# Kernel optimization log

Hardware: AMD Instinct MI355X
Metric: run time of the kernel (lower is better)

Reference implementation:

```python
import jax, jax.numpy as jnp
import numpy as np

M, N = 32, 32
IN_MULT, OUT_MULT = 5, 40
HQ = M * M  # 1024, hidden size of GRU_Q and GRU_Sigma; GRU_S hidden = N*N = 1024


def _l2norm(x):
    # torch F.normalize(p=2, dim=0, eps=1e-12)
    return x / jnp.maximum(jnp.linalg.norm(x), 1e-12)


def _gru(x, h, Wih, Whh, bih, bhh):
    # single-step torch nn.GRU cell, gate order r,z,n
    gi = Wih @ x + bih
    gh = Whh @ h + bhh
    Hh = h.shape[0]
    r = jax.nn.sigmoid(gi[:Hh] + gh[:Hh])
    z = jax.nn.sigmoid(gi[Hh:2 * Hh] + gh[Hh:2 * Hh])
    n = jnp.tanh(gi[2 * Hh:] + r * gh[2 * Hh:])
    return (1.0 - z) * n + z * h


def setup_inputs() -> dict:
    key = jax.random.key(0)
    ks = iter(jax.random.split(key, 48))

    def rn(shape, scale=1.0):
        return jax.random.normal(next(ks), shape, dtype=jnp.float32) * jnp.float32(scale)

    def w(o, i):
        return rn((o, i), 1.0 / np.sqrt(i))

    d_in_sigma = HQ + M * IN_MULT          # 1184
    d_in_s = N * N + 2 * N * IN_MULT       # 1344
    d_fc2_in = HQ + N * N                  # 2048
    d_fc2_hid = d_fc2_in * OUT_MULT        # 81920
    inp = dict(
        y=rn((N,)),
        m1x_posterior=rn((M, 1)), m1x_posterior_previous=rn((M, 1)),
        m1x_prior_previous=rn((M, 1)), y_previous=rn((N, 1)),
        h_Q=rn((HQ,)), h_Sigma=rn((HQ,)), h_S=rn((N * N,)),
        F=w(M, M), H=w(N, M),
        FC5_w=w(M * IN_MULT, M), FC5_b=rn((M * IN_MULT,), 0.01),
        FC6_w=w(M * IN_MULT, M), FC6_b=rn((M * IN_MULT,), 0.01),
        FC7_w=w(2 * N * IN_MULT, 2 * N), FC7_b=rn((2 * N * IN_MULT,), 0.01),
        GRUQ_Wih=w(3 * HQ, M * IN_MULT), GRUQ_Whh=w(3 * HQ, HQ),
        GRUQ_bih=rn((3 * HQ,), 0.01), GRUQ_bhh=rn((3 * HQ,), 0.01),
        GRUSig_Wih=w(3 * HQ, d_in_sigma), GRUSig_Whh=w(3 * HQ, HQ),
        GRUSig_bih=rn((3 * HQ,), 0.01), GRUSig_bhh=rn((3 * HQ,), 0.01),
        GRUS_Wih=w(3 * N * N, d_in_s), GRUS_Whh=w(3 * N * N, N * N),
        GRUS_bih=rn((3 * N * N,), 0.01), GRUS_bhh=rn((3 * N * N,), 0.01),
        FC1_w=w(N * N, HQ), FC1_b=rn((N * N,), 0.01),
        FC2_w1=w(d_fc2_hid, d_fc2_in), FC2_b1=rn((d_fc2_hid,), 0.01),
        FC2_w2=w(N * M, d_fc2_hid), FC2_b2=rn((N * M,), 0.01),
        FC3_w=w(M * M, N * N + N * M), FC3_b=rn((M * M,), 0.01),
        FC4_w=w(HQ, HQ + M * M), FC4_b=rn((HQ,), 0.01),
        fix_H_flag=1,
    )
    return inp


def _forward(y, m1x_posterior, m1x_posterior_previous, m1x_prior_previous, y_previous,
             h_Q, h_Sigma, h_S, F, H,
             FC5_w, FC5_b, FC6_w, FC6_b, FC7_w, FC7_b,
             GRUQ_Wih, GRUQ_Whh, GRUQ_bih, GRUQ_bhh,
             GRUSig_Wih, GRUSig_Whh, GRUSig_bih, GRUSig_bhh,
             GRUS_Wih, GRUS_Whh, GRUS_bih, GRUS_bhh,
             FC1_w, FC1_b, FC2_w1, FC2_b1, FC2_w2, FC2_b2,
             FC3_w, FC3_b, FC4_w, FC4_b):
    # step_prior (fix_H_flag=True path: h is linear)
    m1x_prior = F @ m1x_posterior          # [m,1]
    m1y = H @ m1x_prior                    # [n,1]
    # step_KGain_est: feature differences, L2-normalized
    obs_diff = _l2norm(y - y_previous[:, 0])
    obs_innov_diff = _l2norm(y - m1y[:, 0])
    fw_evol_diff = _l2norm(m1x_posterior[:, 0] - m1x_posterior_previous[:, 0])
    fw_update_diff = _l2norm(m1x_posterior[:, 0] - m1x_prior_previous[:, 0])
    # KGain_step (dropout layers are identity in eval)
    out_FC5 = jax.nn.relu(FC5_w @ fw_evol_diff + FC5_b)
    out_Q = _gru(out_FC5, h_Q, GRUQ_Wih, GRUQ_Whh, GRUQ_bih, GRUQ_bhh)
    out_FC6 = jax.nn.relu(FC6_w @ fw_update_diff + FC6_b)
    out_Sigma = _gru(jnp.concatenate([out_Q, out_FC6]), h_Sigma,
                     GRUSig_Wih, GRUSig_Whh, GRUSig_bih, GRUSig_bhh)
    out_FC1 = jax.nn.relu(FC1_w @ out_Sigma + FC1_b)
    out_FC7 = jax.nn.relu(FC7_w @ jnp.concatenate([obs_diff, obs_innov_diff]) + FC7_b)
    out_S = _gru(jnp.concatenate([out_FC1, out_FC7]), h_S,
                 GRUS_Wih, GRUS_Whh, GRUS_bih, GRUS_bhh)
    in_FC2 = jnp.concatenate([out_Sigma, out_S])
    out_FC2 = FC2_w2 @ jax.nn.relu(FC2_w1 @ in_FC2 + FC2_b1) + FC2_b2   # [m*n]
    out_FC3 = jax.nn.relu(FC3_w @ jnp.concatenate([out_S, out_FC2]) + FC3_b)
    out_FC4 = jax.nn.relu(FC4_w @ jnp.concatenate([out_Sigma, out_FC3]) + FC4_b)  # new h_Sigma state
    del out_FC4  # state update only; not part of returned output
    # KNet_step update
    KG = out_FC2.reshape(M, N)
    dy = y[:, None] - m1y
    m1x_posterior_new = m1x_prior + KG @ dy
    return m1x_posterior_new[:, 0]


def reference(y, m1x_posterior, m1x_posterior_previous, m1x_prior_previous, y_previous,
              h_Q, h_Sigma, h_S, F, H,
              FC5_w, FC5_b, FC6_w, FC6_b, FC7_w, FC7_b,
              GRUQ_Wih, GRUQ_Whh, GRUQ_bih, GRUQ_bhh,
              GRUSig_Wih, GRUSig_Whh, GRUSig_bih, GRUSig_bhh,
              GRUS_Wih, GRUS_Whh, GRUS_bih, GRUS_bhh,
              FC1_w, FC1_b, FC2_w1, FC2_b1, FC2_w2, FC2_b2,
              FC3_w, FC3_b, FC4_w, FC4_b, fix_H_flag):
    return _forward(y, m1x_posterior, m1x_posterior_previous, m1x_prior_previous, y_previous,
                    h_Q, h_Sigma, h_S, F, H,
                    FC5_w, FC5_b, FC6_w, FC6_b, FC7_w, FC7_b,
                    GRUQ_Wih, GRUQ_Whh, GRUQ_bih, GRUQ_bhh,
                    GRUSig_Wih, GRUSig_Whh, GRUSig_bih, GRUSig_bhh,
                    GRUS_Wih, GRUS_Whh, GRUS_bih, GRUS_bhh,
                    FC1_w, FC1_b, FC2_w1, FC2_b1, FC2_w2, FC2_b2,
                    FC3_w, FC3_b, FC4_w, FC4_b)
```

## Files before the change

kernel.cpp:

```cpp
#include <hip/hip_runtime.h>
#include <math.h>

#define DEV __device__ __forceinline__

typedef float f4 __attribute__((ext_vector_type(4)));

DEV f4 ntl(const f4* p) { return __builtin_nontemporal_load(p); }

DEV float dot4(f4 w, f4 x) {
    float s = 0.f;
    s = fmaf(w.x, x.x, s); s = fmaf(w.y, x.y, s);
    s = fmaf(w.z, x.z, s); s = fmaf(w.w, x.w, s);
    return s;
}

DEV float wave_reduce(float v) {
    for (int off = 32; off > 0; off >>= 1) v += __shfl_down(v, off);
    return v;
}
DEV float reduce32(float v) {
    for (int off = 16; off > 0; off >>= 1) v += __shfl_xor(v, off);
    return v;
}

#define WS_Q     0
#define WS_FC6   1024
#define WS_SIG   1184
#define WS_FC1   2208
#define WS_FC7   3232
#define WS_S     3552
#define WS_HID   4576
#define WS_DY    86496

template <int K4X>
DEV void gru_row(int row, int t, const float* __restrict__ x,
                 const float* __restrict__ h,
                 const float* __restrict__ Wih, const float* __restrict__ Whh,
                 const float* __restrict__ bih, const float* __restrict__ bhh,
                 float* __restrict__ out) {
    const f4* x4 = (const f4*)x;
    const f4* w0 = (const f4*)Wih + (size_t)row * K4X;
    const f4* w1 = (const f4*)Wih + (size_t)(1024 + row) * K4X;
    const f4* w2 = (const f4*)Wih + (size_t)(2048 + row) * K4X;
    float ai0 = 0.f, ai1 = 0.f, ai2 = 0.f;
    if (K4X >= 256 || t < K4X) {
        f4 xv = x4[t];
        ai0 = dot4(ntl(w0 + t), xv);
        ai1 = dot4(ntl(w1 + t), xv);
        ai2 = dot4(ntl(w2 + t), xv);
    }
    if (K4X > 256) {
        if (t < K4X - 256) {
            int k = 256 + t;
            f4 xv = x4[k];
            ai0 += dot4(ntl(w0 + k), xv);
            ai1 += dot4(ntl(w1 + k), xv);
            ai2 += dot4(ntl(w2 + k), xv);
        }
    }
    const f4* v0 = (const f4*)Whh + (size_t)row * 256;
    const f4* v1 = (const f4*)Whh + (size_t)(1024 + row) * 256;
    const f4* v2 = (const f4*)Whh + (size_t)(2048 + row) * 256;
    f4 hv = ((const f4*)h)[t];
    float ah0 = dot4(ntl(v0 + t), hv);
    float ah1 = dot4(ntl(v1 + t), hv);
    float ah2 = dot4(ntl(v2 + t), hv);
    ai0 = wave_reduce(ai0); ai1 = wave_reduce(ai1); ai2 = wave_reduce(ai2);
    ah0 = wave_reduce(ah0); ah1 = wave_reduce(ah1); ah2 = wave_reduce(ah2);
    __shared__ float red[4][6];
    int w = t >> 6, lane = t & 63;
    if (lane == 0) {
        red[w][0] = ai0; red[w][1] = ai1; red[w][2] = ai2;
        red[w][3] = ah0; red[w][4] = ah1; red[w][5] = ah2;
    }
    __syncthreads();
    if (t == 0) {
        float AI0 = red[0][0] + red[1][0] + red[2][0] + red[3][0];
        float AI1 = red[0][1] + red[1][1] + red[2][1] + red[3][1];
        float AI2 = red[0][2] + red[1][2] + red[2][2] + red[3][2];
        float AH0 = red[0][3] + red[1][3] + red[2][3] + red[3][3];
        float AH1 = red[0][4] + red[1][4] + red[2][4] + red[3][4];
        float AH2 = red[0][5] + red[1][5] + red[2][5] + red[3][5];
        float gr = AI0 + bih[row]        + AH0 + bhh[row];
        float gz = AI1 + bih[row + 1024] + AH1 + bhh[row + 1024];
        float r = 1.f / (1.f + expf(-gr));
        float z = 1.f / (1.f + expf(-gz));
        float n = tanhf(AI2 + bih[row + 2048] + r * (AH2 + bhh[row + 2048]));
        out[row] = (1.f - z) * n + z * h[row];
    }
}

__global__ __launch_bounds__(256) void k_stage1(
        const float* __restrict__ y, const float* __restrict__ y_prev,
        const float* __restrict__ post, const float* __restrict__ post_prev,
        const float* __restrict__ prior_prev,
        const float* __restrict__ F, const float* __restrict__ Hm,
        const float* __restrict__ fc5w, const float* __restrict__ fc5b,
        const float* __restrict__ fc6w, const float* __restrict__ fc6b,
        const float* __restrict__ fc7w, const float* __restrict__ fc7b,
        const float* __restrict__ h_Q,
        const float* __restrict__ Wih, const float* __restrict__ Whh,
        const float* __restrict__ bih, const float* __restrict__ bhh,
        float* __restrict__ ws, float* __restrict__ out) {
    int t = threadIdx.x;
    if (blockIdx.x < 1024) {
        __shared__ __align__(16) float sx[160];
        __shared__ float sd[32];
        __shared__ float sinv;
        if (t < 32) sd[t] = post[t] - post_prev[t];
        __syncthreads();
        if (t < 64) {
            float d = (t < 32) ? sd[t] * sd[t] : 0.f;
            d = wave_reduce(d);
            if (t == 0) sinv = 1.f / fmaxf(sqrtf(d), 1e-12f);
        }
        __syncthreads();
        if (t < 160) {
            float a = 0.f;
#pragma unroll
            for (int j = 0; j < 32; ++j) a = fmaf(fc5w[t * 32 + j], sd[j], a);
            sx[t] = fmaxf(fmaf(a, sinv, fc5b[t]), 0.f);
        }
        __syncthreads();
        gru_row<40>(blockIdx.x, t, sx, h_Q, Wih, Whh, bih, bhh, ws + WS_Q);
    } else if (blockIdx.x == 1024) {
        __shared__ float sd[32];
        __shared__ float sinv;
        if (t < 32) sd[t] = post[t] - prior_prev[t];
        __syncthreads();
        if (t < 64) {
            float d = (t < 32) ? sd[t] * sd[t] : 0.f;
            d = wave_reduce(d);
            if (t == 0) sinv = 1.f / fmaxf(sqrtf(d), 1e-12f);
        }
        __syncthreads();
        if (t < 160) {
            float a = 0.f;
#pragma unroll
            for (int j = 0; j < 32; ++j) a = fmaf(fc6w[t * 32 + j], sd[j], a);
            ws[WS_FC6 + t] = fmaxf(fmaf(a, sinv, fc6b[t]), 0.f);
        }
    } else {
        __shared__ float sp[32], sd0[32], sd1[32];
        __shared__ float sinv0, sinv1;
        if (t < 32) {
            float p = 0.f;
#pragma unroll
            for (int j = 0; j < 32; ++j) p = fmaf(F[t * 32 + j], post[j], p);
            sp[t] = p;
            sd0[t] = y[t] - y_prev[t];
        }
        __syncthreads();
        if (t < 32) {
            float m = 0.f;
#pragma unroll
            for (int j = 0; j < 32; ++j) m = fmaf(Hm[t * 32 + j], sp[j], m);
            float dy = y[t] - m;
            sd1[t] = dy;
            ws[WS_DY + t] = dy;
            out[t] = sp[t];
        }
        __syncthreads();
        if (t < 64) {
            int g = t >> 5, j = t & 31;
            float d = g ? sd1[j] : sd0[j];
            float s = reduce32(d * d);
            if (j == 0) {
                float inv = 1.f / fmaxf(sqrtf(s), 1e-12f);
                if (g) sinv1 = inv; else sinv0 = inv;
            }
        }
        __syncthreads();
        for (int r = t; r < 320; r += 256) {
            float a0 = 0.f, a1 = 0.f;
#pragma unroll
            for (int j = 0; j < 32; ++j) {
                a0 = fmaf(fc7w[r * 64 + j], sd0[j], a0);
                a1 = fmaf(fc7w[r * 64 + 32 + j], sd1[j], a1);
            }
            ws[WS_FC7 + r] = fmaxf(a0 * sinv0 + a1 * sinv1 + fc7b[r], 0.f);
        }
    }
}

__global__ __launch_bounds__(256) void k_stage2(
        const float* __restrict__ h, const float* __restrict__ Wih,
        const float* __restrict__ Whh, const float* __restrict__ bih,
        const float* __restrict__ bhh, float* __restrict__ ws) {
    gru_row<296>(blockIdx.x, threadIdx.x, ws + WS_Q, h, Wih, Whh, bih, bhh, ws + WS_SIG);
}

DEV void w1a_wave(int wid, int t, const float* __restrict__ W1, float* __restrict__ ws) {
    int lane = t & 63;
    const f4* w4 = (const f4*)W1 + (size_t)wid * 512;
    const f4* x4 = (const f4*)(ws + WS_SIG);
    float a0 = 0.f, a1 = 0.f;
#pragma unroll
    for (int i = 0; i < 4; ++i) {
        int k = lane + (i << 6);
        float v = dot4(ntl(w4 + k), x4[k]);
        if (i & 1) a1 += v; else a0 += v;
    }
    float a = wave_reduce(a0 + a1);
    if (lane == 0) ws[WS_HID + wid] = a;
}

__global__ __launch_bounds__(256) void k_stage3(
        const float* __restrict__ W1, const float* __restrict__ fc1w,
        const float* __restrict__ fc1b, float* __restrict__ ws) {
    int t = threadIdx.x;
    if (blockIdx.x < 1024) {
        int row = blockIdx.x;
        const f4* w4 = (const f4*)fc1w + (size_t)row * 256;
        const f4* x4 = (const f4*)(ws + WS_SIG);
        float a = dot4(ntl(w4 + t), x4[t]);
        a = wave_reduce(a);
        __shared__ float s[4];
        if ((t & 63) == 0) s[t >> 6] = a;
        __syncthreads();
        if (t == 0) ws[WS_FC1 + row] = fmaxf(s[0] + s[1] + s[2] + s[3] + fc1b[row], 0.f);
    } else {
        int wid = ((blockIdx.x - 1024) << 2) + (t >> 6);
        w1a_wave(wid, t, W1, ws);
    }
}

__global__ __launch_bounds__(256) void k_stage4(
        const float* __restrict__ W1, const float* __restrict__ h,
        const float* __restrict__ Wih, const float* __restrict__ Whh,
        const float* __restrict__ bih, const float* __restrict__ bhh,
        float* __restrict__ ws) {
    int t = threadIdx.x;
    if (blockIdx.x < 1024) {
        gru_row<336>(blockIdx.x, t, ws + WS_FC1, h, Wih, Whh, bih, bhh, ws + WS_S);
    } else {
        int wid = 40960 + ((blockIdx.x - 1024) << 2) + (t >> 6);
        w1a_wave(wid, t, W1, ws);
    }
}

__global__ __launch_bounds__(256) void k_w1b(
        const float* __restrict__ W1, const float* __restrict__ b1,
        float* __restrict__ ws) {
    int wid = (blockIdx.x << 2) + (threadIdx.x >> 6);
    int lane = threadIdx.x & 63;
    const f4* w4 = (const f4*)W1 + (size_t)wid * 512 + 256;
    const f4* x4 = (const f4*)(ws + WS_S);
    float a0 = 0.f, a1 = 0.f;
#pragma unroll
    for (int i = 0; i < 4; ++i) {
        int k = lane + (i << 6);
        float v = dot4(ntl(w4 + k), x4[k]);
        if (i & 1) a1 += v; else a0 += v;
    }
    float a = wave_reduce(a0 + a1);
    if (lane == 0) ws[WS_HID + wid] = fmaxf(ws[WS_HID + wid] + a + b1[wid], 0.f);
}

__global__ __launch_bounds__(512) void k_w2(
        const float* __restrict__ W2, const float* __restrict__ b2,
        const float* __restrict__ ws, float* __restrict__ out) {
    int row = blockIdx.x;
    int t = threadIdx.x;
    const f4* w4 = (const f4*)W2 + (size_t)row * 20480;
    const f4* x4 = (const f4*)(ws + WS_HID);
    float a0 = 0.f, a1 = 0.f;
#pragma unroll 4
    for (int k = t; k < 20480; k += 512) {
        float v = dot4(ntl(w4 + k), x4[k]);
        if (k & 512) a1 += v; else a0 += v;
    }
    float a = wave_reduce(a0 + a1);
    __shared__ float s[8];
    if ((t & 63) == 0) s[t >> 6] = a;
    __syncthreads();
    if (t == 0) {
        float r = b2[row];
#pragma unroll
        for (int i = 0; i < 8; ++i) r += s[i];
        atomicAdd(&out[row >> 5], r * ws[WS_DY + (row & 31)]);
    }
}

extern "C" void kernel_launch(void* const* d_in, const int* in_sizes, int n_in,
                              void* d_out, int out_size, void* d_ws, size_t ws_size,
                              hipStream_t stream) {
    const float* y          = (const float*)d_in[0];
    const float* post       = (const float*)d_in[1];
    const float* post_prev  = (const float*)d_in[2];
    const float* prior_prev = (const float*)d_in[3];
    const float* y_prev     = (const float*)d_in[4];
    const float* h_Q        = (const float*)d_in[5];
    const float* h_Sigma    = (const float*)d_in[6];
    const float* h_S        = (const float*)d_in[7];
    const float* F          = (const float*)d_in[8];
    const float* Hm         = (const float*)d_in[9];
    const float* FC5_w      = (const float*)d_in[10];
    const float* FC5_b      = (const float*)d_in[11];
    const float* FC6_w      = (const float*)d_in[12];
    const float* FC6_b      = (const float*)d_in[13];
    const float* FC7_w      = (const float*)d_in[14];
    const float* FC7_b      = (const float*)d_in[15];
    const float* GQ_Wih     = (const float*)d_in[16];
    const float* GQ_Whh     = (const float*)d_in[17];
    const float* GQ_bih     = (const float*)d_in[18];
    const float* GQ_bhh     = (const float*)d_in[19];
    const float* GS_Wih     = (const float*)d_in[20];
    const float* GS_Whh     = (const float*)d_in[21];
    const float* GS_bih     = (const float*)d_in[22];
    const float* GS_bhh     = (const float*)d_in[23];
    const float* GU_Wih     = (const float*)d_in[24];
    const float* GU_Whh     = (const float*)d_in[25];
    const float* GU_bih     = (const float*)d_in[26];
    const float* GU_bhh     = (const float*)d_in[27];
    const float* FC1_w      = (const float*)d_in[28];
    const float* FC1_b      = (const float*)d_in[29];
    const float* FC2_w1     = (const float*)d_in[30];
    const float* FC2_b1     = (const float*)d_in[31];
    const float* FC2_w2     = (const float*)d_in[32];
    const float* FC2_b2     = (const float*)d_in[33];

    float* ws = (float*)d_ws;
    float* out = (float*)d_out;

    k_stage1<<<1026, 256, 0, stream>>>(y, y_prev, post, post_prev, prior_prev, F, Hm,
                                       FC5_w, FC5_b, FC6_w, FC6_b, FC7_w, FC7_b,
                                       h_Q, GQ_Wih, GQ_Whh, GQ_bih, GQ_bhh, ws, out);
    k_stage2<<<1024, 256, 0, stream>>>(h_Sigma, GS_Wih, GS_Whh, GS_bih, GS_bhh, ws);
    k_stage3<<<11264, 256, 0, stream>>>(FC2_w1, FC1_w, FC1_b, ws);
    k_stage4<<<11264, 256, 0, stream>>>(FC2_w1, h_S, GU_Wih, GU_Whh, GU_bih, GU_bhh, ws);
    k_w1b<<<20480, 256, 0, stream>>>(FC2_w1, FC2_b1, ws);
    k_w2<<<1024, 512, 0, stream>>>(FC2_w2, FC2_b2, ws, out);
}
```

Before: 181.0 us.

## Hoist GRU hidden-state matvecs into first stage and split input-weight work

```diff
diff --git a/kernel.cpp b/kernel.cpp
--- a/kernel.cpp
+++ b/kernel.cpp
@@ -29,8 +29,11 @@
 #define WS_FC1   2208
 #define WS_FC7   3232
 #define WS_S     3552
-#define WS_HID   4576
-#define WS_DY    86496
+#define WS_AHS   4576
+#define WS_AHU   7648
+#define WS_AIU   10720
+#define WS_HID   13792
+#define WS_DY    95712
 
 template <int K4X>
 DEV void gru_row(int row, int t, const float* __restrict__ x,
@@ -49,15 +52,6 @@
         ai1 = dot4(ntl(w1 + t), xv);
         ai2 = dot4(ntl(w2 + t), xv);
     }
-    if (K4X > 256) {
-        if (t < K4X - 256) {
-            int k = 256 + t;
-            f4 xv = x4[k];
-            ai0 += dot4(ntl(w0 + k), xv);
-            ai1 += dot4(ntl(w1 + k), xv);
-            ai2 += dot4(ntl(w2 + k), xv);
-        }
-    }
     const f4* v0 = (const f4*)Whh + (size_t)row * 256;
     const f4* v1 = (const f4*)Whh + (size_t)(1024 + row) * 256;
     const f4* v2 = (const f4*)Whh + (size_t)(2048 + row) * 256;
@@ -90,6 +84,27 @@
     }
 }
 
+DEV void hh_row(int row, int t, const float* __restrict__ h,
+                const float* __restrict__ Whh, float* __restrict__ dst) {
+    const f4* v0 = (const f4*)Whh + (size_t)row * 256;
+    const f4* v1 = (const f4*)Whh + (size_t)(1024 + row) * 256;
+    const f4* v2 = (const f4*)Whh + (size_t)(2048 + row) * 256;
+    f4 hv = ((const f4*)h)[t];
+    float a0 = dot4(ntl(v0 + t), hv);
+    float a1 = dot4(ntl(v1 + t), hv);
+    float a2 = dot4(ntl(v2 + t), hv);
+    a0 = wave_reduce(a0); a1 = wave_reduce(a1); a2 = wave_reduce(a2);
+    __shared__ float red[4][3];
+    int w = t >> 6, lane = t & 63;
+    if (lane == 0) { red[w][0] = a0; red[w][1] = a1; red[w][2] = a2; }
+    __syncthreads();
+    if (t == 0) {
+        dst[row]        = red[0][0] + red[1][0] + red[2][0] + red[3][0];
+        dst[row + 1024] = red[0][1] + red[1][1] + red[2][1] + red[3][1];
+        dst[row + 2048] = red[0][2] + red[1][2] + red[2][2] + red[3][2];
+    }
+}
+
 __global__ __launch_bounds__(256) void k_stage1(
         const float* __restrict__ y, const float* __restrict__ y_prev,
         const float* __restrict__ post, const float* __restrict__ post_prev,
@@ -98,12 +113,15 @@
         const float* __restrict__ fc5w, const float* __restrict__ fc5b,
         const float* __restrict__ fc6w, const float* __restrict__ fc6b,
         const float* __restrict__ fc7w, const float* __restrict__ fc7b,
-        const float* __restrict__ h_Q,
+        const float* __restrict__ h_Q, const float* __restrict__ h_Sig,
+        const float* __restrict__ h_S,
         const float* __restrict__ Wih, const float* __restrict__ Whh,
         const float* __restrict__ bih, const float* __restrict__ bhh,
+        const float* __restrict__ WhhSig, const float* __restrict__ WhhS,
         float* __restrict__ ws, float* __restrict__ out) {
     int t = threadIdx.x;
-    if (blockIdx.x < 1024) {
+    int b = blockIdx.x;
+    if (b < 1024) {
         __shared__ __align__(16) float sx[160];
         __shared__ float sd[32];
         __shared__ float sinv;
@@ -122,8 +140,8 @@
             sx[t] = fmaxf(fmaf(a, sinv, fc5b[t]), 0.f);
         }
         __syncthreads();
-        gru_row<40>(blockIdx.x, t, sx, h_Q, Wih, Whh, bih, bhh, ws + WS_Q);
-    } else if (blockIdx.x == 1024) {
+        gru_row<40>(b, t, sx, h_Q, Wih, Whh, bih, bhh, ws + WS_Q);
+    } else if (b == 1024) {
         __shared__ float sd[32];
         __shared__ float sinv;
         if (t < 32) sd[t] = post[t] - prior_prev[t];
@@ -140,7 +158,7 @@
             for (int j = 0; j < 32; ++j) a = fmaf(fc6w[t * 32 + j], sd[j], a);
             ws[WS_FC6 + t] = fmaxf(fmaf(a, sinv, fc6b[t]), 0.f);
         }
-    } else {
+    } else if (b == 1025) {
         __shared__ float sp[32], sd0[32], sd1[32];
         __shared__ float sinv0, sinv1;
         if (t < 32) {
@@ -180,14 +198,53 @@
             }
             ws[WS_FC7 + r] = fmaxf(a0 * sinv0 + a1 * sinv1 + fc7b[r], 0.f);
         }
+    } else if (b < 2050) {
+        hh_row(b - 1026, t, h_Sig, WhhSig, ws + WS_AHS);
+    } else {
+        hh_row(b - 2050, t, h_S, WhhS, ws + WS_AHU);
     }
 }
 
 __global__ __launch_bounds__(256) void k_stage2(
         const float* __restrict__ h, const float* __restrict__ Wih,
-        const float* __restrict__ Whh, const float* __restrict__ bih,
-        const float* __restrict__ bhh, float* __restrict__ ws) {
-    gru_row<296>(blockIdx.x, threadIdx.x, ws + WS_Q, h, Wih, Whh, bih, bhh, ws + WS_SIG);
+        const float* __restrict__ bih, const float* __restrict__ bhh,
+        float* __restrict__ ws) {
+    int row = blockIdx.x;
+    int t = threadIdx.x;
+    const f4* x4 = (const f4*)(ws + WS_Q);
+    const f4* w0 = (const f4*)Wih + (size_t)row * 296;
+    const f4* w1 = (const f4*)Wih + (size_t)(1024 + row) * 296;
+    const f4* w2 = (const f4*)Wih + (size_t)(2048 + row) * 296;
+    f4 xv = x4[t];
+    float a0 = dot4(ntl(w0 + t), xv);
+    float a1 = dot4(ntl(w1 + t), xv);
+    float a2 = dot4(ntl(w2 + t), xv);
+    if (t < 40) {
+        int k = 256 + t;
+        f4 xw = x4[k];
+        a0 += dot4(ntl(w0 + k), xw);
+        a1 += dot4(ntl(w1 + k), xw);
+        a2 += dot4(ntl(w2 + k), xw);
+    }
+    a0 = wave_reduce(a0); a1 = wave_reduce(a1); a2 = wave_reduce(a2);
+    __shared__ float red[4][3];
+    int w = t >> 6, lane = t & 63;
+    if (lane == 0) { red[w][0] = a0; red[w][1] = a1; red[w][2] = a2; }
+    __syncthreads();
+    if (t == 0) {
+        float AI0 = red[0][0] + red[1][0] + red[2][0] + red[3][0];
+        float AI1 = red[0][1] + red[1][1] + red[2][1] + red[3][1];
+        float AI2 = red[0][2] + red[1][2] + red[2][2] + red[3][2];
+        float AH0 = ws[WS_AHS + row];
+        float AH1 = ws[WS_AHS + row + 1024];
+        float AH2 = ws[WS_AHS + row + 2048];
+        float gr = AI0 + bih[row]        + AH0 + bhh[row];
+        float gz = AI1 + bih[row + 1024] + AH1 + bhh[row + 1024];
+        float r = 1.f / (1.f + expf(-gr));
+        float z = 1.f / (1.f + expf(-gz));
+        float n = tanhf(AI2 + bih[row + 2048] + r * (AH2 + bhh[row + 2048]));
+        ws[WS_SIG + row] = (1.f - z) * n + z * h[row];
+    }
 }
 
 DEV void w1a_wave(int wid, int t, const float* __restrict__ W1, float* __restrict__ ws) {
@@ -207,18 +264,38 @@
 
 __global__ __launch_bounds__(256) void k_stage3(
         const float* __restrict__ W1, const float* __restrict__ fc1w,
-        const float* __restrict__ fc1b, float* __restrict__ ws) {
+        const float* __restrict__ fc1b, const float* __restrict__ WihS,
+        float* __restrict__ ws) {
     int t = threadIdx.x;
     if (blockIdx.x < 1024) {
         int row = blockIdx.x;
         const f4* w4 = (const f4*)fc1w + (size_t)row * 256;
         const f4* x4 = (const f4*)(ws + WS_SIG);
-        float a = dot4(ntl(w4 + t), x4[t]);
-        a = wave_reduce(a);
-        __shared__ float s[4];
-        if ((t & 63) == 0) s[t >> 6] = a;
-        __syncthreads();
-        if (t == 0) ws[WS_FC1 + row] = fmaxf(s[0] + s[1] + s[2] + s[3] + fc1b[row], 0.f);
+        float afc = dot4(ntl(w4 + t), x4[t]);
+        const f4* xs4 = (const f4*)(ws + WS_FC7);
+        float u0 = 0.f, u1 = 0.f, u2 = 0.f;
+        if (t < 80) {
+            f4 xv = xs4[t];
+            const f4* s0 = (const f4*)WihS + (size_t)row * 336 + 256;
+            const f4* s1 = (const f4*)WihS + (size_t)(1024 + row) * 336 + 256;
+            const f4* s2 = (const f4*)WihS + (size_t)(2048 + row) * 336 + 256;
+            u0 = dot4(ntl(s0 + t), xv);
+            u1 = dot4(ntl(s1 + t), xv);
+            u2 = dot4(ntl(s2 + t), xv);
+        }
+        afc = wave_reduce(afc);
+        u0 = wave_reduce(u0); u1 = wave_reduce(u1); u2 = wave_reduce(u2);
+        __shared__ float red[4][4];
+        int w = t >> 6, lane = t & 63;
+        if (lane == 0) { red[w][0] = afc; red[w][1] = u0; red[w][2] = u1; red[w][3] = u2; }
+        __syncthreads();
+        if (t == 0) {
+            ws[WS_FC1 + row] = fmaxf(red[0][0] + red[1][0] + red[2][0] + red[3][0]
+                                     + fc1b[row], 0.f);
+            ws[WS_AIU + row]        = red[0][1] + red[1][1] + red[2][1] + red[3][1];
+            ws[WS_AIU + row + 1024] = red[0][2] + red[1][2] + red[2][2] + red[3][2];
+            ws[WS_AIU + row + 2048] = red[0][3] + red[1][3] + red[2][3] + red[3][3];
+        }
     } else {
         int wid = ((blockIdx.x - 1024) << 2) + (t >> 6);
         w1a_wave(wid, t, W1, ws);
@@ -227,12 +304,39 @@
 
 __global__ __launch_bounds__(256) void k_stage4(
         const float* __restrict__ W1, const float* __restrict__ h,
-        const float* __restrict__ Wih, const float* __restrict__ Whh,
+        const float* __restrict__ WihS,
         const float* __restrict__ bih, const float* __restrict__ bhh,
         float* __restrict__ ws) {
     int t = threadIdx.x;
     if (blockIdx.x < 1024) {
-        gru_row<336>(blockIdx.x, t, ws + WS_FC1, h, Wih, Whh, bih, bhh, ws + WS_S);
+        int row = blockIdx.x;
+        const f4* x4 = (const f4*)(ws + WS_FC1);
+        const f4* w0 = (const f4*)WihS + (size_t)row * 336;
+        const f4* w1 = (const f4*)WihS + (size_t)(1024 + row) * 336;
+        const f4* w2 = (const f4*)WihS + (size_t)(2048 + row) * 336;
+        f4 xv = x4[t];
+        float a0 = dot4(ntl(w0 + t), xv);
+        float a1 = dot4(ntl(w1 + t), xv);
+        float a2 = dot4(ntl(w2 + t), xv);
+        a0 = wave_reduce(a0); a1 = wave_reduce(a1); a2 = wave_reduce(a2);
+        __shared__ float red[4][3];
+        int w = t >> 6, lane = t & 63;
+        if (lane == 0) { red[w][0] = a0; red[w][1] = a1; red[w][2] = a2; }
+        __syncthreads();
+        if (t == 0) {
+            float AI0 = red[0][0] + red[1][0] + red[2][0] + red[3][0] + ws[WS_AIU + row];
+            float AI1 = red[0][1] + red[1][1] + red[2][1] + red[3][1] + ws[WS_AIU + row + 1024];
+            float AI2 = red[0][2] + red[1][2] + red[2][2] + red[3][2] + ws[WS_AIU + row + 2048];
+            float AH0 = ws[WS_AHU + row];
+            float AH1 = ws[WS_AHU + row + 1024];
+            float AH2 = ws[WS_AHU + row + 2048];
+            float gr = AI0 + bih[row]        + AH0 + bhh[row];
+            float gz = AI1 + bih[row + 1024] + AH1 + bhh[row + 1024];
+            float r = 1.f / (1.f + expf(-gr));
+            float z = 1.f / (1.f + expf(-gz));
+            float n = tanhf(AI2 + bih[row + 2048] + r * (AH2 + bhh[row + 2048]));
+            ws[WS_S + row] = (1.f - z) * n + z * h[row];
+        }
     } else {
         int wid = 40960 + ((blockIdx.x - 1024) << 2) + (t >> 6);
         w1a_wave(wid, t, W1, ws);
@@ -323,12 +427,14 @@
     float* ws = (float*)d_ws;
     float* out = (float*)d_out;
 
-    k_stage1<<<1026, 256, 0, stream>>>(y, y_prev, post, post_prev, prior_prev, F, Hm,
+    k_stage1<<<3074, 256, 0, stream>>>(y, y_prev, post, post_prev, prior_prev, F, Hm,
                                        FC5_w, FC5_b, FC6_w, FC6_b, FC7_w, FC7_b,
-                                       h_Q, GQ_Wih, GQ_Whh, GQ_bih, GQ_bhh, ws, out);
-    k_stage2<<<1024, 256, 0, stream>>>(h_Sigma, GS_Wih, GS_Whh, GS_bih, GS_bhh, ws);
-    k_stage3<<<11264, 256, 0, stream>>>(FC2_w1, FC1_w, FC1_b, ws);
-    k_stage4<<<11264, 256, 0, stream>>>(FC2_w1, h_S, GU_Wih, GU_Whh, GU_bih, GU_bhh, ws);
+                                       h_Q, h_Sigma, h_S,
+                                       GQ_Wih, GQ_Whh, GQ_bih, GQ_bhh,
+                                       GS_Whh, GU_Whh, ws, out);
+    k_stage2<<<1024, 256, 0, stream>>>(h_Sigma, GS_Wih, GS_bih, GS_bhh, ws);
+    k_stage3<<<11264, 256, 0, stream>>>(FC2_w1, FC1_w, FC1_b, GU_Wih, ws);
+    k_stage4<<<11264, 256, 0, stream>>>(FC2_w1, h_S, GU_Wih, GU_bih, GU_bhh, ws);
     k_w1b<<<20480, 256, 0, stream>>>(FC2_w1, FC2_b1, ws);
     k_w2<<<1024, 512, 0, stream>>>(FC2_w2, FC2_b2, ws, out);
 }
```

New measurement: 179.9 us. About the same (-0.6%).
